# Kernel optimization log

Hardware: AMD Instinct MI355X
Metric: run time of the kernel (lower is better)

## Reference

```python
import jax, jax.numpy as jnp
import numpy as np


def setup_inputs() -> dict:
    key = jax.random.key(0)
    kq, kk, kv, kiq, kik = jax.random.split(key, 5)
    B, H, S, D = 2, 16, 4096, 64
    NSQ = 2048  # round(0.5 * S)
    NSK = 2048  # round(0.5 * S)
    Q = jax.random.normal(kq, (B, H, S, D), dtype=jnp.float32)
    K = jax.random.normal(kk, (B, H, S, D), dtype=jnp.float32)
    V = jax.random.normal(kv, (B, H, S, D), dtype=jnp.float32)
    mask = jnp.ones((B, S), dtype=jnp.float32)
    sample_idx_q = jnp.sort(jax.random.randint(kiq, (NSQ,), 0, S, dtype=jnp.int32))
    sample_idx_k = jax.random.randint(kik, (NSK,), 0, S, dtype=jnp.int32)
    return {"Q": Q, "K": K, "V": V, "mask": mask,
            "sample_idx_q": sample_idx_q, "sample_idx_k": sample_idx_k}


def reference(Q, K, V, mask, sample_idx_q, sample_idx_k):
    # Q,K,V: [B,H,S,D]; sample_idx_q sorted int [NSQ]; sample_idx_k int [NSK]
    S = Q.shape[-2]
    nsq = sample_idx_q.shape[0]
    nsk = sample_idx_k.shape[0]
    Qs = Q[:, :, sample_idx_q, :]            # [B,H,NSQ,D]
    Vs = V[:, :, sample_idx_k, :]            # [B,H,NSK,D]
    # NOTE: original code computes K's softmax from Q (faithful to source bug):
    Qsm = jax.nn.softmax(Qs, axis=-1)        # softmax over head_dim
    Ksm = jax.nn.softmax(Qsm, axis=-2)       # softmax over sampled seq dim
    # dot = K^T @ V : [B,H,D,D]  (requires NSQ == NSK, as in source)
    dot = jnp.einsum('bhsd,bhse->bhde', Ksm, Vs)
    ac = jnp.einsum('bhsd,bhde->bhse', Qsm, dot)  # [B,H,NSQ,D]
    scale = (S * S) / (nsq * nsk)
    ac = scale * ac + (S / nsk) * Vs
    # Serial duplicate-merge + scatter == segmented sum over duplicate q indices,
    # written into a zero tensor at the unique sampled positions.
    attn = jnp.zeros_like(V).at[:, :, sample_idx_q, :].add(ac)
    return attn
```

## Files before the change

kernel.cpp:

```cpp
#include <hip/hip_runtime.h>

constexpr int S    = 4096;
constexpr int D    = 64;
constexpr int NSQ  = 2048;
constexpr int BH   = 32;
constexpr int SD   = S * D;

constexpr int SPA  = 32;
constexpr int RPBA = NSQ / SPA;
constexpr int ITA  = 4;
constexpr int PEA  = 66;

constexpr int SPC  = 32;
constexpr int RPBC = NSQ / SPC;
constexpr int PQ   = 68;

using f32x16 = __attribute__((ext_vector_type(16))) float;
using s16x8  = __attribute__((ext_vector_type(8)))  short;

#define DEV static __device__ __forceinline__

DEV unsigned short f2bf(float f) {
    unsigned x = __builtin_bit_cast(unsigned, f);
    x += 0x7fffu + ((x >> 16) & 1u);
    return (unsigned short)(x >> 16);
}

DEV s16x8 load_frag(const unsigned short* p) {
    const unsigned* u = (const unsigned*)p;
    union { unsigned w[4]; s16x8 v; } r;
    r.w[0] = u[0]; r.w[1] = u[1]; r.w[2] = u[2]; r.w[3] = u[3];
    return r.v;
}

__global__ __launch_bounds__(256) void
kA(const float* __restrict__ Q, const float* __restrict__ V,
   const int* __restrict__ iq, const int* __restrict__ ik,
   float* __restrict__ Mp, float* __restrict__ Cp,
   unsigned short* __restrict__ Qsw) {
    __shared__ unsigned short Et[64 * PEA];
    __shared__ unsigned short Vt[64 * PEA];
    __shared__ float Cl[4][256];
    __shared__ int iqL[RPBA], ikL[RPBA];

    const int bh   = blockIdx.x / SPA;
    const int sp   = blockIdx.x % SPA;
    const int lane = threadIdx.x & 63;
    const int wave = threadIdx.x >> 6;
    const int rq   = lane >> 4;
    const int c    = lane & 15;

    const int rbase = sp * RPBA;
    if (threadIdx.x < RPBA) {
        iqL[threadIdx.x] = iq[rbase + threadIdx.x];
        ikL[threadIdx.x] = ik[rbase + threadIdx.x];
    }
    __syncthreads();

    const float* Qb = Q + (size_t)bh * SD;
    const float* Vb = V + (size_t)bh * SD;

    float c4[4] = {0.f, 0.f, 0.f, 0.f};
    #pragma unroll
    for (int it = 0; it < ITA; ++it) {
        const int sl = wave * 16 + it * 4 + rq;
        const int qi = iqL[sl];
        const int ki = ikL[sl];
        const float4 qv = *(const float4*)&Qb[qi * D + 4 * c];
        const float4 vv = *(const float4*)&Vb[ki * D + 4 * c];
        const float e0 = __expf(qv.x), e1 = __expf(qv.y),
                    e2 = __expf(qv.z), e3 = __expf(qv.w);
        float s = (e0 + e1) + (e2 + e3);
        s += __shfl_xor(s, 1); s += __shfl_xor(s, 2);
        s += __shfl_xor(s, 4); s += __shfl_xor(s, 8);
        const float inv = 1.0f / s;
        const float q0 = e0 * inv, q1 = e1 * inv, q2 = e2 * inv, q3 = e3 * inv;
        const float E0 = __expf(q0), E1 = __expf(q1),
                    E2 = __expf(q2), E3 = __expf(q3);
        c4[0] += E0; c4[1] += E1; c4[2] += E2; c4[3] += E3;
        Et[(4 * c + 0) * PEA + sl] = f2bf(E0);
        Et[(4 * c + 1) * PEA + sl] = f2bf(E1);
        Et[(4 * c + 2) * PEA + sl] = f2bf(E2);
        Et[(4 * c + 3) * PEA + sl] = f2bf(E3);
        Vt[(4 * c + 0) * PEA + sl] = f2bf(vv.x);
        Vt[(4 * c + 1) * PEA + sl] = f2bf(vv.y);
        Vt[(4 * c + 2) * PEA + sl] = f2bf(vv.z);
        Vt[(4 * c + 3) * PEA + sl] = f2bf(vv.w);
        uint2 pk;
        pk.x = (unsigned)f2bf(q0) | ((unsigned)f2bf(q1) << 16);
        pk.y = (unsigned)f2bf(q2) | ((unsigned)f2bf(q3) << 16);
        *(uint2*)&Qsw[((size_t)bh * NSQ + rbase + sl) * 64 + 4 * c] = pk;
    }
    Cl[wave][lane * 4 + 0] = c4[0];
    Cl[wave][lane * 4 + 1] = c4[1];
    Cl[wave][lane * 4 + 2] = c4[2];
    Cl[wave][lane * 4 + 3] = c4[3];
    __syncthreads();

    const int d0 = (wave & 1) * 32, n0 = (wave >> 1) * 32;
    const int m  = lane & 31, h = lane >> 5;
    f32x16 acc = {0,0,0,0,0,0,0,0,0,0,0,0,0,0,0,0};
    #pragma unroll
    for (int t = 0; t < RPBA / 16; ++t) {
        s16x8 a = load_frag(&Et[(d0 + m) * PEA + t * 16 + h * 8]);
        s16x8 b = load_frag(&Vt[(n0 + m) * PEA + t * 16 + h * 8]);
        acc = __builtin_amdgcn_mfma_f32_32x32x16_bf16(a, b, acc, 0, 0, 0);
    }
    float* Mb = Mp + ((size_t)bh * SPA + sp) * 4096;
    #pragma unroll
    for (int r = 0; r < 16; ++r) {
        const int row = (r & 3) + 8 * (r >> 2) + 4 * h;
        Mb[(d0 + row) * 64 + n0 + m] = acc[r];
    }
    if (wave == 0) {
        const int cc = lane >> 2, j = lane & 3;
        float cs = 0.f;
        #pragma unroll
        for (int w = 0; w < 4; ++w)
            #pragma unroll
            for (int r = 0; r < 4; ++r)
                cs += Cl[w][(16 * r + cc) * 4 + j];
        Cp[((size_t)bh * SPA + sp) * 64 + lane] = cs;
    }
}

__global__ __launch_bounds__(256) void
kB(const float* __restrict__ Mp, const float* __restrict__ Cp,
   unsigned short* __restrict__ Gtw) {
    __shared__ float Cf[64];
    const int bh = blockIdx.x >> 2;
    const int qr = blockIdx.x & 3;

    if (threadIdx.x < 64) {
        float cs = 0.f;
        #pragma unroll 8
        for (int p = 0; p < SPA; ++p)
            cs += Cp[((size_t)bh * SPA + p) * 64 + threadIdx.x];
        Cf[threadIdx.x] = cs;
    }
    __syncthreads();

    const int l = qr * 1024 + threadIdx.x * 4;
    const int d = l >> 6;
    const float* MpB = Mp + (size_t)bh * SPA * 4096;
    float4 ms = {0.f, 0.f, 0.f, 0.f};
    #pragma unroll 8
    for (int p = 0; p < SPA; ++p) {
        const float4 t = *(const float4*)&MpB[p * 4096 + l];
        ms.x += t.x; ms.y += t.y; ms.z += t.z; ms.w += t.w;
    }
    const float g = 4.0f / Cf[d];
    uint2 pk;
    pk.x = (unsigned)f2bf(ms.x * g) | ((unsigned)f2bf(ms.y * g) << 16);
    pk.y = (unsigned)f2bf(ms.z * g) | ((unsigned)f2bf(ms.w * g) << 16);
    *(uint2*)&Gtw[(size_t)bh * 4096 + l] = pk;
}

__global__ __launch_bounds__(256) void
kC(const float* __restrict__ V,
   const int* __restrict__ iq, const int* __restrict__ ik,
   const unsigned short* __restrict__ Qsw, const unsigned short* __restrict__ Gtw,
   float* __restrict__ out) {
    __shared__ unsigned short Qs[RPBC * PQ];
    __shared__ unsigned short Gt[64 * PQ];
    __shared__ int iqL[RPBC], ikL[RPBC];

    const int bh   = blockIdx.x / SPC;
    const int sp   = blockIdx.x % SPC;
    const int lane = threadIdx.x & 63;
    const int wave = threadIdx.x >> 6;
    const int rbase = sp * RPBC;

    if (threadIdx.x < RPBC) {
        iqL[threadIdx.x] = iq[rbase + threadIdx.x];
        ikL[threadIdx.x] = ik[rbase + threadIdx.x];
    }

    {
        const int l0 = threadIdx.x * 16;
        const int d  = l0 >> 6;
        const uint4 w0 = *(const uint4*)&Gtw[(size_t)bh * 4096 + l0];
        const uint4 w1 = *(const uint4*)&Gtw[(size_t)bh * 4096 + l0 + 8];
        const unsigned wv[8] = {w0.x, w0.y, w0.z, w0.w, w1.x, w1.y, w1.z, w1.w};
        const int e0 = l0 & 63;
        #pragma unroll
        for (int j = 0; j < 8; ++j) {
            Gt[(e0 + 2 * j + 0) * PQ + d] = (unsigned short)(wv[j] & 0xffffu);
            Gt[(e0 + 2 * j + 1) * PQ + d] = (unsigned short)(wv[j] >> 16);
        }
    }
    {
        const int l0  = threadIdx.x * 16;
        const int row = l0 >> 6, col = l0 & 63;
        const uint4 w0 = *(const uint4*)&Qsw[((size_t)bh * NSQ + rbase) * 64 + l0];
        const uint4 w1 = *(const uint4*)&Qsw[((size_t)bh * NSQ + rbase) * 64 + l0 + 8];
        *(uint2*)&Qs[row * PQ + col + 0] = make_uint2(w0.x, w0.y);
        *(uint2*)&Qs[row * PQ + col + 4] = make_uint2(w0.z, w0.w);
        *(uint2*)&Qs[row * PQ + col + 8] = make_uint2(w1.x, w1.y);
        *(uint2*)&Qs[row * PQ + col + 12] = make_uint2(w1.z, w1.w);
    }
    __syncthreads();

    const float* Vb = V + (size_t)bh * SD;
    float*       Ob = out + (size_t)bh * SD;

    const int m0 = (wave & 1) * 32, n0 = (wave >> 1) * 32;
    const int m  = lane & 31, h = lane >> 5;
    f32x16 acc;
    #pragma unroll
    for (int r = 0; r < 16; ++r) {
        const int row = (r & 3) + 8 * (r >> 2) + 4 * h;
        const int ki  = ikL[m0 + row];
        acc[r] = 2.0f * Vb[ki * D + n0 + m];
    }
    #pragma unroll
    for (int t = 0; t < RPBC / 16; ++t) {
        s16x8 a = load_frag(&Qs[(m0 + m) * PQ + t * 16 + h * 8]);
        s16x8 b = load_frag(&Gt[(n0 + m) * PQ + t * 16 + h * 8]);
        acc = __builtin_amdgcn_mfma_f32_32x32x16_bf16(a, b, acc, 0, 0, 0);
    }
    #pragma unroll
    for (int r = 0; r < 16; ++r) {
        const int row = (r & 3) + 8 * (r >> 2) + 4 * h;
        const int qi  = iqL[m0 + row];
        atomicAdd(&Ob[qi * D + n0 + m], acc[r]);
    }
}

extern "C" void kernel_launch(void* const* d_in, const int* in_sizes, int n_in,
                              void* d_out, int out_size, void* d_ws, size_t ws_size,
                              hipStream_t stream) {
    const float* Q  = (const float*)d_in[0];
    const float* V  = (const float*)d_in[2];
    const int*   iq = (const int*)d_in[4];
    const int*   ik = (const int*)d_in[5];
    float*       out = (float*)d_out;

    float*          Mp  = (float*)d_ws;
    float*          Cp  = Mp + (size_t)BH * SPA * 4096;
    unsigned short* Qsw = (unsigned short*)(Cp + (size_t)BH * SPA * 64);
    unsigned short* Gtw = Qsw + (size_t)BH * NSQ * 64;

    hipMemsetAsync(d_out, 0, (size_t)out_size * sizeof(float), stream);
    kA<<<BH * SPA, 256, 0, stream>>>(Q, V, iq, ik, Mp, Cp, Qsw);
    kB<<<BH * 4, 256, 0, stream>>>(Mp, Cp, Gtw);
    kC<<<BH * SPC, 256, 0, stream>>>(V, iq, ik, Qsw, Gtw, out);
}
```

Before: 156.3 us.

## Fuse three kernels and memset into one cooperative kernel with grid syncs

Result: slower. 367.2 us (+135.0%).

```diff
diff --git a/kernel.cpp b/kernel.cpp
--- a/kernel.cpp
+++ b/kernel.cpp
@@ -1,4 +1,7 @@
 #include <hip/hip_runtime.h>
+#include <hip/hip_cooperative_groups.h>
+
+namespace cg = cooperative_groups;
 
 constexpr int S    = 4096;
 constexpr int D    = 64;
@@ -7,12 +10,8 @@
 constexpr int SD   = S * D;
 
 constexpr int SPA  = 32;
-constexpr int RPBA = NSQ / SPA;
-constexpr int ITA  = 4;
+constexpr int RPB  = NSQ / SPA;
 constexpr int PEA  = 66;
-
-constexpr int SPC  = 32;
-constexpr int RPBC = NSQ / SPC;
 constexpr int PQ   = 68;
 
 using f32x16 = __attribute__((ext_vector_type(16))) float;
@@ -25,7 +24,10 @@
     x += 0x7fffu + ((x >> 16) & 1u);
     return (unsigned short)(x >> 16);
 }
-
+DEV float bf2f(unsigned short u) {
+    unsigned x = (unsigned)u << 16;
+    return __builtin_bit_cast(float, x);
+}
 DEV s16x8 load_frag(const unsigned short* p) {
     const unsigned* u = (const unsigned*)p;
     union { unsigned w[4]; s16x8 v; } r;
@@ -33,15 +35,16 @@
     return r.v;
 }
 
-__global__ __launch_bounds__(256) void
-kA(const float* __restrict__ Q, const float* __restrict__ V,
-   const int* __restrict__ iq, const int* __restrict__ ik,
-   float* __restrict__ Mp, float* __restrict__ Cp,
-   unsigned short* __restrict__ Qsw) {
-    __shared__ unsigned short Et[64 * PEA];
+__global__ __launch_bounds__(256, 4) void
+kFused(const float* __restrict__ Q, const float* __restrict__ V,
+       const int* __restrict__ iq, const int* __restrict__ ik,
+       float* __restrict__ Mp, float* __restrict__ Cp,
+       unsigned short* __restrict__ Gtw, float* __restrict__ out) {
+    __shared__ unsigned short Qs[RPB * PQ];
     __shared__ unsigned short Vt[64 * PEA];
+    __shared__ unsigned short EtGt[64 * PQ];
     __shared__ float Cl[4][256];
-    __shared__ int iqL[RPBA], ikL[RPBA];
+    __shared__ int iqL[RPB], ikL[RPB];
 
     const int bh   = blockIdx.x / SPA;
     const int sp   = blockIdx.x % SPA;
@@ -49,9 +52,17 @@
     const int wave = threadIdx.x >> 6;
     const int rq   = lane >> 4;
     const int c    = lane & 15;
-
-    const int rbase = sp * RPBA;
-    if (threadIdx.x < RPBA) {
+    const int rbase = sp * RPB;
+
+    cg::grid_group grid = cg::this_grid();
+
+    {
+        float4 z = {0.f, 0.f, 0.f, 0.f};
+        float4* ob = (float4*)out + (size_t)blockIdx.x * 2048;
+        #pragma unroll
+        for (int j = 0; j < 8; ++j) ob[j * 256 + threadIdx.x] = z;
+    }
+    if (threadIdx.x < RPB) {
         iqL[threadIdx.x] = iq[rbase + threadIdx.x];
         ikL[threadIdx.x] = ik[rbase + threadIdx.x];
     }
@@ -62,7 +73,7 @@
 
     float c4[4] = {0.f, 0.f, 0.f, 0.f};
     #pragma unroll
-    for (int it = 0; it < ITA; ++it) {
+    for (int it = 0; it < 4; ++it) {
         const int sl = wave * 16 + it * 4 + rq;
         const int qi = iqL[sl];
         const int ki = ikL[sl];
@@ -78,10 +89,10 @@
         const float E0 = __expf(q0), E1 = __expf(q1),
                     E2 = __expf(q2), E3 = __expf(q3);
         c4[0] += E0; c4[1] += E1; c4[2] += E2; c4[3] += E3;
-        Et[(4 * c + 0) * PEA + sl] = f2bf(E0);
-        Et[(4 * c + 1) * PEA + sl] = f2bf(E1);
-        Et[(4 * c + 2) * PEA + sl] = f2bf(E2);
-        Et[(4 * c + 3) * PEA + sl] = f2bf(E3);
+        EtGt[(4 * c + 0) * PEA + sl] = f2bf(E0);
+        EtGt[(4 * c + 1) * PEA + sl] = f2bf(E1);
+        EtGt[(4 * c + 2) * PEA + sl] = f2bf(E2);
+        EtGt[(4 * c + 3) * PEA + sl] = f2bf(E3);
         Vt[(4 * c + 0) * PEA + sl] = f2bf(vv.x);
         Vt[(4 * c + 1) * PEA + sl] = f2bf(vv.y);
         Vt[(4 * c + 2) * PEA + sl] = f2bf(vv.z);
@@ -89,7 +100,7 @@
         uint2 pk;
         pk.x = (unsigned)f2bf(q0) | ((unsigned)f2bf(q1) << 16);
         pk.y = (unsigned)f2bf(q2) | ((unsigned)f2bf(q3) << 16);
-        *(uint2*)&Qsw[((size_t)bh * NSQ + rbase + sl) * 64 + 4 * c] = pk;
+        *(uint2*)&Qs[sl * PQ + 4 * c] = pk;
     }
     Cl[wave][lane * 4 + 0] = c4[0];
     Cl[wave][lane * 4 + 1] = c4[1];
@@ -97,133 +108,89 @@
     Cl[wave][lane * 4 + 3] = c4[3];
     __syncthreads();
 
-    const int d0 = (wave & 1) * 32, n0 = (wave >> 1) * 32;
     const int m  = lane & 31, h = lane >> 5;
-    f32x16 acc = {0,0,0,0,0,0,0,0,0,0,0,0,0,0,0,0};
-    #pragma unroll
-    for (int t = 0; t < RPBA / 16; ++t) {
-        s16x8 a = load_frag(&Et[(d0 + m) * PEA + t * 16 + h * 8]);
-        s16x8 b = load_frag(&Vt[(n0 + m) * PEA + t * 16 + h * 8]);
-        acc = __builtin_amdgcn_mfma_f32_32x32x16_bf16(a, b, acc, 0, 0, 0);
-    }
-    float* Mb = Mp + ((size_t)bh * SPA + sp) * 4096;
-    #pragma unroll
-    for (int r = 0; r < 16; ++r) {
-        const int row = (r & 3) + 8 * (r >> 2) + 4 * h;
-        Mb[(d0 + row) * 64 + n0 + m] = acc[r];
-    }
-    if (wave == 0) {
-        const int cc = lane >> 2, j = lane & 3;
-        float cs = 0.f;
-        #pragma unroll
-        for (int w = 0; w < 4; ++w)
+    {
+        const int d0 = (wave & 1) * 32, n0 = (wave >> 1) * 32;
+        f32x16 acc = {0,0,0,0,0,0,0,0,0,0,0,0,0,0,0,0};
+        #pragma unroll
+        for (int t = 0; t < RPB / 16; ++t) {
+            s16x8 a = load_frag(&EtGt[(d0 + m) * PEA + t * 16 + h * 8]);
+            s16x8 b = load_frag(&Vt[(n0 + m) * PEA + t * 16 + h * 8]);
+            acc = __builtin_amdgcn_mfma_f32_32x32x16_bf16(a, b, acc, 0, 0, 0);
+        }
+        float* Mb = Mp + ((size_t)bh * SPA + sp) * 4096;
+        #pragma unroll
+        for (int r = 0; r < 16; ++r) {
+            const int row = (r & 3) + 8 * (r >> 2) + 4 * h;
+            Mb[(d0 + row) * 64 + n0 + m] = acc[r];
+        }
+        if (wave == 0) {
+            const int cc = lane >> 2, j = lane & 3;
+            float cs = 0.f;
             #pragma unroll
-            for (int r = 0; r < 4; ++r)
-                cs += Cl[w][(16 * r + cc) * 4 + j];
-        Cp[((size_t)bh * SPA + sp) * 64 + lane] = cs;
-    }
-}
-
-__global__ __launch_bounds__(256) void
-kB(const float* __restrict__ Mp, const float* __restrict__ Cp,
-   unsigned short* __restrict__ Gtw) {
-    __shared__ float Cf[64];
-    const int bh = blockIdx.x >> 2;
-    const int qr = blockIdx.x & 3;
-
-    if (threadIdx.x < 64) {
+            for (int w = 0; w < 4; ++w)
+                #pragma unroll
+                for (int r = 0; r < 4; ++r)
+                    cs += Cl[w][(16 * r + cc) * 4 + j];
+            Cp[((size_t)bh * SPA + sp) * 64 + lane] = cs;
+        }
+    }
+
+    grid.sync();
+
+    if (threadIdx.x < 128) {
+        const int l = sp * 128 + threadIdx.x;
+        const int d = l >> 6;
+        const float* MpB = Mp + (size_t)bh * SPA * 4096;
+        float ms = 0.f;
+        #pragma unroll 8
+        for (int p = 0; p < SPA; ++p)
+            ms += MpB[p * 4096 + l];
         float cs = 0.f;
         #pragma unroll 8
         for (int p = 0; p < SPA; ++p)
-            cs += Cp[((size_t)bh * SPA + p) * 64 + threadIdx.x];
-        Cf[threadIdx.x] = cs;
-    }
-    __syncthreads();
-
-    const int l = qr * 1024 + threadIdx.x * 4;
-    const int d = l >> 6;
-    const float* MpB = Mp + (size_t)bh * SPA * 4096;
-    float4 ms = {0.f, 0.f, 0.f, 0.f};
-    #pragma unroll 8
-    for (int p = 0; p < SPA; ++p) {
-        const float4 t = *(const float4*)&MpB[p * 4096 + l];
-        ms.x += t.x; ms.y += t.y; ms.z += t.z; ms.w += t.w;
-    }
-    const float g = 4.0f / Cf[d];
-    uint2 pk;
-    pk.x = (unsigned)f2bf(ms.x * g) | ((unsigned)f2bf(ms.y * g) << 16);
-    pk.y = (unsigned)f2bf(ms.z * g) | ((unsigned)f2bf(ms.w * g) << 16);
-    *(uint2*)&Gtw[(size_t)bh * 4096 + l] = pk;
-}
-
-__global__ __launch_bounds__(256) void
-kC(const float* __restrict__ V,
-   const int* __restrict__ iq, const int* __restrict__ ik,
-   const unsigned short* __restrict__ Qsw, const unsigned short* __restrict__ Gtw,
-   float* __restrict__ out) {
-    __shared__ unsigned short Qs[RPBC * PQ];
-    __shared__ unsigned short Gt[64 * PQ];
-    __shared__ int iqL[RPBC], ikL[RPBC];
-
-    const int bh   = blockIdx.x / SPC;
-    const int sp   = blockIdx.x % SPC;
-    const int lane = threadIdx.x & 63;
-    const int wave = threadIdx.x >> 6;
-    const int rbase = sp * RPBC;
-
-    if (threadIdx.x < RPBC) {
-        iqL[threadIdx.x] = iq[rbase + threadIdx.x];
-        ikL[threadIdx.x] = ik[rbase + threadIdx.x];
-    }
+            cs += Cp[((size_t)bh * SPA + p) * 64 + d];
+        Gtw[(size_t)bh * 4096 + l] = f2bf(4.0f * ms / cs);
+    }
+
+    grid.sync();
 
     {
         const int l0 = threadIdx.x * 16;
         const int d  = l0 >> 6;
+        const int e0 = l0 & 63;
         const uint4 w0 = *(const uint4*)&Gtw[(size_t)bh * 4096 + l0];
         const uint4 w1 = *(const uint4*)&Gtw[(size_t)bh * 4096 + l0 + 8];
         const unsigned wv[8] = {w0.x, w0.y, w0.z, w0.w, w1.x, w1.y, w1.z, w1.w};
-        const int e0 = l0 & 63;
         #pragma unroll
         for (int j = 0; j < 8; ++j) {
-            Gt[(e0 + 2 * j + 0) * PQ + d] = (unsigned short)(wv[j] & 0xffffu);
-            Gt[(e0 + 2 * j + 1) * PQ + d] = (unsigned short)(wv[j] >> 16);
-        }
-    }
-    {
-        const int l0  = threadIdx.x * 16;
-        const int row = l0 >> 6, col = l0 & 63;
-        const uint4 w0 = *(const uint4*)&Qsw[((size_t)bh * NSQ + rbase) * 64 + l0];
-        const uint4 w1 = *(const uint4*)&Qsw[((size_t)bh * NSQ + rbase) * 64 + l0 + 8];
-        *(uint2*)&Qs[row * PQ + col + 0] = make_uint2(w0.x, w0.y);
-        *(uint2*)&Qs[row * PQ + col + 4] = make_uint2(w0.z, w0.w);
-        *(uint2*)&Qs[row * PQ + col + 8] = make_uint2(w1.x, w1.y);
-        *(uint2*)&Qs[row * PQ + col + 12] = make_uint2(w1.z, w1.w);
+            EtGt[(e0 + 2 * j + 0) * PQ + d] = (unsigned short)(wv[j] & 0xffffu);
+            EtGt[(e0 + 2 * j + 1) * PQ + d] = (unsigned short)(wv[j] >> 16);
+        }
     }
     __syncthreads();
 
-    const float* Vb = V + (size_t)bh * SD;
-    float*       Ob = out + (size_t)bh * SD;
-
-    const int m0 = (wave & 1) * 32, n0 = (wave >> 1) * 32;
-    const int m  = lane & 31, h = lane >> 5;
-    f32x16 acc;
-    #pragma unroll
-    for (int r = 0; r < 16; ++r) {
-        const int row = (r & 3) + 8 * (r >> 2) + 4 * h;
-        const int ki  = ikL[m0 + row];
-        acc[r] = 2.0f * Vb[ki * D + n0 + m];
-    }
-    #pragma unroll
-    for (int t = 0; t < RPBC / 16; ++t) {
-        s16x8 a = load_frag(&Qs[(m0 + m) * PQ + t * 16 + h * 8]);
-        s16x8 b = load_frag(&Gt[(n0 + m) * PQ + t * 16 + h * 8]);
-        acc = __builtin_amdgcn_mfma_f32_32x32x16_bf16(a, b, acc, 0, 0, 0);
-    }
-    #pragma unroll
-    for (int r = 0; r < 16; ++r) {
-        const int row = (r & 3) + 8 * (r >> 2) + 4 * h;
-        const int qi  = iqL[m0 + row];
-        atomicAdd(&Ob[qi * D + n0 + m], acc[r]);
+    {
+        const int m0 = (wave & 1) * 32, n0 = (wave >> 1) * 32;
+        f32x16 acc;
+        #pragma unroll
+        for (int r = 0; r < 16; ++r) {
+            const int row = (r & 3) + 8 * (r >> 2) + 4 * h;
+            acc[r] = 2.0f * bf2f(Vt[(n0 + m) * PEA + (m0 + row)]);
+        }
+        #pragma unroll
+        for (int t = 0; t < RPB / 16; ++t) {
+            s16x8 a = load_frag(&Qs[(m0 + m) * PQ + t * 16 + h * 8]);
+            s16x8 b = load_frag(&EtGt[(n0 + m) * PQ + t * 16 + h * 8]);
+            acc = __builtin_amdgcn_mfma_f32_32x32x16_bf16(a, b, acc, 0, 0, 0);
+        }
+        float* Ob = out + (size_t)bh * SD;
+        #pragma unroll
+        for (int r = 0; r < 16; ++r) {
+            const int row = (r & 3) + 8 * (r >> 2) + 4 * h;
+            const int qi  = iqL[m0 + row];
+            atomicAdd(&Ob[qi * D + n0 + m], acc[r]);
+        }
     }
 }
 
@@ -238,11 +205,10 @@
 
     float*          Mp  = (float*)d_ws;
     float*          Cp  = Mp + (size_t)BH * SPA * 4096;
-    unsigned short* Qsw = (unsigned short*)(Cp + (size_t)BH * SPA * 64);
-    unsigned short* Gtw = Qsw + (size_t)BH * NSQ * 64;
-
-    hipMemsetAsync(d_out, 0, (size_t)out_size * sizeof(float), stream);
-    kA<<<BH * SPA, 256, 0, stream>>>(Q, V, iq, ik, Mp, Cp, Qsw);
-    kB<<<BH * 4, 256, 0, stream>>>(Mp, Cp, Gtw);
-    kC<<<BH * SPC, 256, 0, stream>>>(V, iq, ik, Qsw, Gtw, out);
-}
+    unsigned short* Gtw = (unsigned short*)(Cp + (size_t)BH * SPA * 64);
+
+    void* args[] = {(void*)&Q, (void*)&V, (void*)&iq, (void*)&ik,
+                    (void*)&Mp, (void*)&Cp, (void*)&Gtw, (void*)&out};
+    hipLaunchCooperativeKernel((void*)kFused, dim3(BH * SPA), dim3(256),
+                               args, 0, stream);
+}
```
